# Optimization experiments

Measured on AMD Instinct MI355X. Metric: run time of the kernel, lower is better.

## Reference

```python
import jax, jax.numpy as jnp
import numpy as np

NUM_HEADS = 16


def setup_inputs() -> dict:
    key = jax.random.key(0)
    ks = jax.random.split(key, 7)
    B, S, H = 4, 1024, 1024
    s = 0.02
    return {
        "x": jax.random.normal(ks[0], (B, S, H), dtype=jnp.float32),
        "Wq": jax.random.normal(ks[1], (H, H), dtype=jnp.float32) * s,
        "bq": jax.random.normal(ks[2], (H,), dtype=jnp.float32) * s,
        "Wk": jax.random.normal(ks[3], (H, H), dtype=jnp.float32) * s,
        "bk": jax.random.normal(ks[4], (H,), dtype=jnp.float32) * s,
        "Wv": jax.random.normal(ks[5], (H, H), dtype=jnp.float32) * s,
        "bv": jax.random.normal(ks[6], (H,), dtype=jnp.float32) * s,
    }


def _split_heads(y, num_heads):
    # rearrange 'b s (h c) -> h b s c'
    b, s, hid = y.shape
    c = hid // num_heads
    return y.reshape(b, s, num_heads, c).transpose(2, 0, 1, 3)


def reference(x, Wq, bq, Wk, bk, Wv, bv):
    h = NUM_HEADS
    head_size = x.shape[-1] // h
    # torch Linear: y = x @ W.T + b
    q = _split_heads(x @ Wq.T + bq, h)  # [h,b,s,c]
    k = _split_heads(x @ Wk.T + bk, h)
    v = _split_heads(x @ Wv.T + bv, h)
    scores = jnp.einsum('hbfc,hbtc->hbft', q, k) / jnp.sqrt(
        jnp.asarray(head_size, x.dtype))
    patterns = jax.nn.softmax(scores, axis=-1)  # softmax over t
    # NOTE: faithful to source, contracts over f (query axis) per
    # einsum('hbft,hbfc->hbtc', patterns, value)
    av = jnp.einsum('hbft,hbfc->hbtc', patterns, v)  # [h,b,t,c]
    # rearrange 'h b s c -> b s (c h)'  (channel-major interleave)
    out = av.transpose(1, 2, 3, 0)  # [b,s,c,h]
    b, s, c, hh = out.shape
    return out.reshape(b, s, c * hh)
```

## Files before the change

### kernel.cpp

```cpp
#include <hip/hip_runtime.h>
#include <hip/hip_bf16.h>

typedef short bf16x8 __attribute__((ext_vector_type(8)));
typedef short bf16x4 __attribute__((ext_vector_type(4)));
typedef float f32x4 __attribute__((ext_vector_type(4)));
typedef unsigned short u16;

#define MFMA32(a, b, c) __builtin_amdgcn_mfma_f32_16x16x32_bf16(a, b, c, 0, 0, 0)

#if defined(__has_builtin)
#if __has_builtin(__builtin_amdgcn_mfma_f32_16x16x16bf16_1k)
#define HAVE_MFMA16 1
#define MFMA16(a, b, c) __builtin_amdgcn_mfma_f32_16x16x16bf16_1k(a, b, c, 0, 0, 0)
#endif
#endif
#ifndef HAVE_MFMA16
static __device__ inline f32x4 mfma16_asm(bf16x4 a, bf16x4 b, f32x4 c) {
    f32x4 d;
    asm volatile("v_mfma_f32_16x16x16_bf16 %0, %1, %2, %3\n\ts_nop 7\n\ts_nop 7"
                 : "=v"(d) : "v"(a), "v"(b), "v"(c));
    return d;
}
#define MFMA16(a, b, c) mfma16_asm(a, b, c)
#endif

__device__ inline float fexp2(float x) {
#if defined(__has_builtin) && __has_builtin(__builtin_amdgcn_exp2f)
    return __builtin_amdgcn_exp2f(x);
#else
    return exp2f(x);
#endif
}

__device__ inline u16 f2bf(float f) {
    unsigned u = __float_as_uint(f);
    unsigned r = (u + 0x7fffu + ((u >> 16) & 1u)) >> 16;
    return (u16)r;
}

__device__ inline float bf2f(u16 v) {
    return __uint_as_float(((unsigned)v) << 16);
}

__device__ inline void gload_lds16(const void* g, void* l) {
    __builtin_amdgcn_global_load_lds(
        (const __attribute__((address_space(1))) void*)g,
        (__attribute__((address_space(3))) void*)l, 16, 0, 0);
}

#define BARRIER() __builtin_amdgcn_s_barrier()

__device__ inline int swz(int row, int colbyte) {
    return row * 128 + (colbyte ^ ((row & 7) << 4));
}

__device__ inline void stage8k_512(const u16* __restrict__ g, int gstride,
                                   u16* lds, int tid) {
    int o = tid * 16;
    int row = o >> 7;
    int colb = (o & 127) ^ ((row & 7) << 4);
    gload_lds16(g + row * gstride + (colb >> 1), (char*)lds + o);
}

__device__ inline void stage16k_256(const u16* __restrict__ g, int gstride,
                                    u16* lds, int tid) {
#pragma unroll
    for (int j = 0; j < 4; j++) {
        int o = (tid + j * 256) * 16;
        int row = o >> 7;
        int colb = (o & 127) ^ ((row & 7) << 4);
        gload_lds16(g + row * gstride + (colb >> 1), (char*)lds + o);
    }
}

__global__ void k_convert(const float* __restrict__ src, u16* __restrict__ dst, int n) {
    int i = (blockIdx.x * blockDim.x + threadIdx.x) * 4;
    if (i < n) {
        float4 v = *reinterpret_cast<const float4*>(src + i);
        ushort4 o;
        o.x = f2bf(v.x); o.y = f2bf(v.y); o.z = f2bf(v.z); o.w = f2bf(v.w);
        *reinterpret_cast<ushort4*>(dst + i) = o;
    }
}

__global__ void k_convert3(const float* __restrict__ s0, const float* __restrict__ s1,
                           const float* __restrict__ s2, u16* __restrict__ dst) {
    const float* s = (blockIdx.y == 0) ? s0 : ((blockIdx.y == 1) ? s1 : s2);
    int i = (blockIdx.x * blockDim.x + threadIdx.x) * 4;
    float4 v = *reinterpret_cast<const float4*>(s + i);
    ushort4 o;
    o.x = f2bf(v.x); o.y = f2bf(v.y); o.z = f2bf(v.z); o.w = f2bf(v.w);
    *reinterpret_cast<ushort4*>(dst + blockIdx.y * 1048576 + i) = o;
}

__global__ __launch_bounds__(256, 3) void k_proj(
    const u16* __restrict__ xb, const u16* __restrict__ wb,
    const float* __restrict__ bq, const float* __restrict__ bk, const float* __restrict__ bv,
    u16* __restrict__ outQ, u16* __restrict__ outK, u16* __restrict__ outVt)
{
    __shared__ __align__(16) u16 As[8192];
    __shared__ __align__(16) u16 Bs[8192];
    const int tid = threadIdx.x;
    const int lane = tid & 63;
    const int w = tid >> 6;
    const int bid = blockIdx.x;
    const int xcd = bid & 7, idx = bid >> 3;
    const int mg = xcd & 3, ng = xcd >> 2;
    const int m0 = (mg * 8 + (idx & 7)) * 128;
    const int nfull = ng * 12 + (idx >> 3);
    const int widx = nfull >> 3;
    const int n0 = (nfull & 7) * 128;
    const u16* W = wb + widx * 1024 * 1024;
    const float* bias = (widx == 0) ? bq : ((widx == 1) ? bk : bv);

    const int wm = (w >> 1) * 64, wn = (w & 1) * 64;
    const int lm = lane & 15, lg = lane >> 4;

    f32x4 zero = {0.f, 0.f, 0.f, 0.f};
    f32x4 acc[4][4];
#pragma unroll
    for (int m = 0; m < 4; m++)
#pragma unroll
        for (int n = 0; n < 4; n++) acc[m][n] = zero;

    for (int it = 0; it < 16; ++it) {
        stage16k_256(xb + m0 * 1024 + it * 64, 1024, As, tid);
        stage16k_256(W + n0 * 1024 + it * 64, 1024, Bs, tid);
        __syncthreads();
        const char* Ab = (const char*)As;
        const char* Bb = (const char*)Bs;
#pragma unroll
        for (int kk = 0; kk < 2; kk++) {
            bf16x8 a[4], b[4];
#pragma unroll
            for (int m = 0; m < 4; m++)
                a[m] = *(const bf16x8*)(Ab + swz(wm + m * 16 + lm, kk * 64 + lg * 16));
#pragma unroll
            for (int n = 0; n < 4; n++)
                b[n] = *(const bf16x8*)(Bb + swz(wn + n * 16 + lm, kk * 64 + lg * 16));
#pragma unroll
            for (int m = 0; m < 4; m++)
#pragma unroll
                for (int n = 0; n < 4; n++)
                    acc[m][n] = MFMA32(a[m], b[n], acc[m][n]);
        }
        __syncthreads();
    }

#pragma unroll
    for (int n = 0; n < 4; n++) {
        int col = n0 + wn + n * 16 + lm;
        float bz = bias[col];
        int h = col >> 6, c = col & 63;
#pragma unroll
        for (int m = 0; m < 4; m++) {
#pragma unroll
            for (int r = 0; r < 4; r++) {
                int row = m0 + wm + m * 16 + lg * 4 + r;
                float v = acc[m][n][r] + bz;
                int bb = row >> 10, s = row & 1023;
                int hb = h * 4 + bb;
                if (widx == 0) {
                    outQ[(hb * 1024 + s) * 64 + c] = f2bf(v * 0.18033688011112042f);
                } else if (widx == 1) {
                    outK[(hb * 1024 + s) * 64 + c] = f2bf(v);
                } else {
                    outVt[(hb * 64 + c) * 1024 + s] = f2bf(v);
                }
            }
        }
    }
}

__global__ __launch_bounds__(512, 2) void k_stats(
    const u16* __restrict__ Q, const u16* __restrict__ K, float* __restrict__ linv_out)
{
    __shared__ __align__(16) u16 sK[2][4096];
    const int bid = blockIdx.x;
    const int hb = (bid & 7) * 8 + ((bid >> 3) & 7);
    const int fb = (bid >> 6) * 256;
    const int tid = threadIdx.x, lane = tid & 63, w = tid >> 6;
    const int lm = lane & 15, lg = lane >> 4;
    const u16* Qh = Q + hb * 65536;
    const u16* Kh = K + hb * 65536;

    bf16x8 a[2][2];
#pragma unroll
    for (int fg = 0; fg < 2; fg++) {
        const u16* qp = &Qh[(fb + w * 32 + fg * 16 + lm) * 64 + lg * 8];
        a[fg][0] = *(const bf16x8*)qp;
        a[fg][1] = *(const bf16x8*)(qp + 32);
    }

    float lrun[2][4] = {{0.f, 0.f, 0.f, 0.f}, {0.f, 0.f, 0.f, 0.f}};

    stage8k_512(Kh, 64, sK[0], tid);
    int cur = 0;
    for (int it = 0; it < 16; ++it) {
        if (it < 15) {
            stage8k_512(Kh + (it + 1) * 64 * 64, 64, sK[cur ^ 1], tid);
            asm volatile("s_waitcnt vmcnt(1)" ::: "memory");
        } else {
            asm volatile("s_waitcnt vmcnt(0)" ::: "memory");
        }
        BARRIER();
        const char* base = (const char*)sK[cur];
#pragma unroll
        for (int n = 0; n < 4; n++) {
            int r = n * 16 + lm;
            bf16x8 b0 = *(const bf16x8*)(base + swz(r, lg * 16));
            bf16x8 b1 = *(const bf16x8*)(base + swz(r, 64 + lg * 16));
#pragma unroll
            for (int fg = 0; fg < 2; fg++) {
                f32x4 z = {0.f, 0.f, 0.f, 0.f};
                z = MFMA32(a[fg][0], b0, z);
                z = MFMA32(a[fg][1], b1, z);
                lrun[fg][0] += fexp2(z[0]);
                lrun[fg][1] += fexp2(z[1]);
                lrun[fg][2] += fexp2(z[2]);
                lrun[fg][3] += fexp2(z[3]);
            }
        }
        BARRIER();
        cur ^= 1;
    }
#pragma unroll
    for (int fg = 0; fg < 2; fg++) {
#pragma unroll
        for (int r = 0; r < 4; r++) {
            float s = lrun[fg][r];
            s += __shfl_xor(s, 1);
            s += __shfl_xor(s, 2);
            s += __shfl_xor(s, 4);
            s += __shfl_xor(s, 8);
            if (lm == 0)
                linv_out[hb * 1024 + fb + w * 32 + fg * 16 + lg * 4 + r] = 1.0f / s;
        }
    }
}

__global__ __launch_bounds__(512, 2) void k_av(
    const u16* __restrict__ Q, const u16* __restrict__ K, const u16* __restrict__ Vt,
    const float* __restrict__ linv, u16* __restrict__ av_sb)
{
    __shared__ __align__(16) u16 sQ[2][4096];
    __shared__ __align__(16) u16 sV[2][4096];
    __shared__ __align__(16) float linv_lds[1024];
    const int bid = blockIdx.x;
    const int hb = (bid & 7) * 8 + ((bid >> 3) & 7);
    const int tb = (bid >> 6) * 256;
    const int tid = threadIdx.x, lane = tid & 63, w = tid >> 6;
    const int lm = lane & 15, lg = lane >> 4;
    const u16* Qh = Q + hb * 65536;
    const u16* Kh = K + hb * 65536;
    const u16* Vh = Vt + hb * 65536;
    const float* lh = linv + hb * 1024;

    bf16x8 bK[2][2];
#pragma unroll
    for (int tg = 0; tg < 2; tg++) {
        const u16* kp = &Kh[(tb + w * 32 + tg * 16 + lm) * 64 + lg * 8];
        bK[tg][0] = *(const bf16x8*)kp;
        bK[tg][1] = *(const bf16x8*)(kp + 32);
    }

    f32x4 zero = {0.f, 0.f, 0.f, 0.f};
    f32x4 accv[2][4];
#pragma unroll
    for (int tg = 0; tg < 2; tg++)
#pragma unroll
        for (int m = 0; m < 4; m++) accv[tg][m] = zero;

    stage8k_512(Qh, 64, sQ[0], tid);
    stage8k_512(Vh, 1024, sV[0], tid);
    *reinterpret_cast<float2*>(&linv_lds[tid * 2]) =
        *reinterpret_cast<const float2*>(&lh[tid * 2]);
    __syncthreads();

    int cur = 0;
    for (int it = 0; it < 16; ++it) {
        if (it < 15) {
            int fn = (it + 1) * 64;
            stage8k_512(Qh + fn * 64, 64, sQ[cur ^ 1], tid);
            stage8k_512(Vh + fn, 1024, sV[cur ^ 1], tid);
            asm volatile("s_waitcnt vmcnt(2)" ::: "memory");
        } else {
            asm volatile("s_waitcnt vmcnt(0)" ::: "memory");
        }
        if (it > 0) BARRIER();
        const char* Qb = (const char*)sQ[cur];
        const char* Vb = (const char*)sV[cur];
        const int fc = it * 64;

        bf16x4 afrag[2][4];
#pragma unroll
        for (int mq = 0; mq < 4; mq++) {
            bf16x8 aq0 = *(const bf16x8*)(Qb + swz(mq * 16 + lm, lg * 16));
            bf16x8 aq1 = *(const bf16x8*)(Qb + swz(mq * 16 + lm, 64 + lg * 16));
            float4 lv = *reinterpret_cast<const float4*>(&linv_lds[fc + mq * 16 + lg * 4]);
#pragma unroll
            for (int tg = 0; tg < 2; tg++) {
                f32x4 z = {0.f, 0.f, 0.f, 0.f};
                z = MFMA32(aq0, bK[tg][0], z);
                z = MFMA32(aq1, bK[tg][1], z);
                union { __hip_bfloat162 h2[2]; bf16x4 v4; } u;
                u.h2[0] = __float22bfloat162_rn(
                    make_float2(fexp2(z[0]) * lv.x, fexp2(z[1]) * lv.y));
                u.h2[1] = __float22bfloat162_rn(
                    make_float2(fexp2(z[2]) * lv.z, fexp2(z[3]) * lv.w));
                afrag[tg][mq] = u.v4;
            }
        }
#pragma unroll
        for (int m = 0; m < 4; m++) {
#pragma unroll
            for (int kc = 0; kc < 4; kc++) {
                bf16x4 bv = *(const bf16x4*)(Vb + swz(m * 16 + lm, kc * 32 + lg * 8));
#pragma unroll
                for (int tg = 0; tg < 2; tg++)
                    accv[tg][m] = MFMA16(afrag[tg][kc], bv, accv[tg][m]);
            }
        }
        BARRIER();
        cur ^= 1;
    }

#pragma unroll
    for (int tg = 0; tg < 2; tg++) {
#pragma unroll
        for (int m = 0; m < 4; m++) {
#pragma unroll
            for (int r = 0; r < 4; r++) {
                int t = tb + w * 32 + tg * 16 + lg * 4 + r;
                av_sb[hb * 65536 + t * 64 + m * 16 + lm] = f2bf(accv[tg][m][r]);
            }
        }
    }
}

__global__ __launch_bounds__(256) void k_interleave(
    const u16* __restrict__ av_sb, float* __restrict__ out)
{
    const int bid = blockIdx.x;
    const int bb = bid >> 7, ts = (bid & 127) * 8;
    const int c = threadIdx.x & 63, tl = threadIdx.x >> 6;
#pragma unroll
    for (int p = 0; p < 2; p++) {
        int t = ts + p * 4 + tl;
        float4 w[4];
#pragma unroll
        for (int q = 0; q < 4; q++) {
#pragma unroll
            for (int j = 0; j < 4; j++) {
                int h = q * 4 + j;
                ((float*)&w[q])[j] = bf2f(av_sb[((h * 4 + bb) * 1024 + t) * 64 + c]);
            }
        }
        float4* dst = (float4*)&out[(bb * 1024 + t) * 1024 + c * 16];
        dst[0] = w[0]; dst[1] = w[1]; dst[2] = w[2]; dst[3] = w[3];
    }
}

extern "C" void kernel_launch(void* const* d_in, const int* in_sizes, int n_in,
                              void* d_out, int out_size, void* d_ws, size_t ws_size,
                              hipStream_t stream) {
    const float* x  = (const float*)d_in[0];
    const float* Wq = (const float*)d_in[1];
    const float* bq = (const float*)d_in[2];
    const float* Wk = (const float*)d_in[3];
    const float* bk = (const float*)d_in[4];
    const float* Wv = (const float*)d_in[5];
    const float* bv = (const float*)d_in[6];
    float* out = (float*)d_out;
    char* ws = (char*)d_ws;

    u16* xb = (u16*)ws;
    u16* wb = (u16*)(ws + (8u << 20));
    u16* Qb = (u16*)(ws + (14u << 20));
    u16* Kb = (u16*)(ws + (22u << 20));
    u16* Vt = (u16*)(ws + (30u << 20));
    float* linv = (float*)(ws + (38u << 20));
    u16* av_sb = (u16*)ws;

    k_convert<<<4096, 256, 0, stream>>>(x, xb, 4096 * 1024);
    k_convert3<<<dim3(1024, 3), 256, 0, stream>>>(Wq, Wk, Wv, wb);
    k_proj<<<768, 256, 0, stream>>>(xb, wb, bq, bk, bv, Qb, Kb, Vt);
    k_stats<<<256, 512, 0, stream>>>(Qb, Kb, linv);
    k_av<<<256, 512, 0, stream>>>(Qb, Kb, Vt, linv, av_sb);
    k_interleave<<<512, 256, 0, stream>>>(av_sb, out);
}
```

Before: 103.8 us.

## Merge convert kernels, shrink projection N-tile, set MFMA priority, relayout AV buffer

Merges the x and weight bf16 conversions into one launch. Halves the projection GEMM N-tile to 64 and doubles the grid to 1536 blocks, raising the occupancy hint to 6 so more waves can hide latency. Adds s_setprio around the MFMA loop in the attention-value kernel, and stores AV output in a [b][t][h][c] layout so the interleave kernel reads contiguously. The smaller tile lowers reuse of the A tile and adds more global loads of x per output.

```diff
diff --git a/kernel.cpp b/kernel.cpp
--- a/kernel.cpp
+++ b/kernel.cpp
@@ -73,33 +73,48 @@
     }
 }
 
-__global__ void k_convert(const float* __restrict__ src, u16* __restrict__ dst, int n) {
-    int i = (blockIdx.x * blockDim.x + threadIdx.x) * 4;
-    if (i < n) {
-        float4 v = *reinterpret_cast<const float4*>(src + i);
-        ushort4 o;
-        o.x = f2bf(v.x); o.y = f2bf(v.y); o.z = f2bf(v.z); o.w = f2bf(v.w);
-        *reinterpret_cast<ushort4*>(dst + i) = o;
-    }
-}
-
-__global__ void k_convert3(const float* __restrict__ s0, const float* __restrict__ s1,
-                           const float* __restrict__ s2, u16* __restrict__ dst) {
-    const float* s = (blockIdx.y == 0) ? s0 : ((blockIdx.y == 1) ? s1 : s2);
-    int i = (blockIdx.x * blockDim.x + threadIdx.x) * 4;
+__device__ inline void stage8k_256(const u16* __restrict__ g, int gstride,
+                                   u16* lds, int tid) {
+#pragma unroll
+    for (int j = 0; j < 2; j++) {
+        int o = (tid + j * 256) * 16;
+        int row = o >> 7;
+        int colb = (o & 127) ^ ((row & 7) << 4);
+        gload_lds16(g + row * gstride + (colb >> 1), (char*)lds + o);
+    }
+}
+
+__global__ void k_convert_all(const float* __restrict__ x,
+                              const float* __restrict__ w0, const float* __restrict__ w1,
+                              const float* __restrict__ w2,
+                              u16* __restrict__ xb, u16* __restrict__ wb) {
+    const int bid = blockIdx.x;
+    const float* s;
+    u16* d;
+    int i;
+    if (bid < 4096) {
+        s = x; d = xb;
+        i = bid * 1024 + threadIdx.x * 4;
+    } else {
+        int wsec = (bid - 4096) >> 10;
+        int boff = (bid - 4096) & 1023;
+        s = (wsec == 0) ? w0 : ((wsec == 1) ? w1 : w2);
+        d = wb + wsec * 1048576;
+        i = boff * 1024 + threadIdx.x * 4;
+    }
     float4 v = *reinterpret_cast<const float4*>(s + i);
     ushort4 o;
     o.x = f2bf(v.x); o.y = f2bf(v.y); o.z = f2bf(v.z); o.w = f2bf(v.w);
-    *reinterpret_cast<ushort4*>(dst + blockIdx.y * 1048576 + i) = o;
-}
-
-__global__ __launch_bounds__(256, 3) void k_proj(
+    *reinterpret_cast<ushort4*>(d + i) = o;
+}
+
+__global__ __launch_bounds__(256, 6) void k_proj(
     const u16* __restrict__ xb, const u16* __restrict__ wb,
     const float* __restrict__ bq, const float* __restrict__ bk, const float* __restrict__ bv,
     u16* __restrict__ outQ, u16* __restrict__ outK, u16* __restrict__ outVt)
 {
     __shared__ __align__(16) u16 As[8192];
-    __shared__ __align__(16) u16 Bs[8192];
+    __shared__ __align__(16) u16 Bs[4096];
     const int tid = threadIdx.x;
     const int lane = tid & 63;
     const int w = tid >> 6;
@@ -107,48 +122,48 @@
     const int xcd = bid & 7, idx = bid >> 3;
     const int mg = xcd & 3, ng = xcd >> 2;
     const int m0 = (mg * 8 + (idx & 7)) * 128;
-    const int nfull = ng * 12 + (idx >> 3);
-    const int widx = nfull >> 3;
-    const int n0 = (nfull & 7) * 128;
+    const int nfull = ng * 24 + (idx >> 3);
+    const int widx = nfull >> 4;
+    const int n0 = (nfull & 15) * 64;
     const u16* W = wb + widx * 1024 * 1024;
     const float* bias = (widx == 0) ? bq : ((widx == 1) ? bk : bv);
 
-    const int wm = (w >> 1) * 64, wn = (w & 1) * 64;
+    const int wm = (w >> 1) * 64, wn = (w & 1) * 32;
     const int lm = lane & 15, lg = lane >> 4;
 
     f32x4 zero = {0.f, 0.f, 0.f, 0.f};
-    f32x4 acc[4][4];
+    f32x4 acc[4][2];
 #pragma unroll
     for (int m = 0; m < 4; m++)
 #pragma unroll
-        for (int n = 0; n < 4; n++) acc[m][n] = zero;
+        for (int n = 0; n < 2; n++) acc[m][n] = zero;
 
     for (int it = 0; it < 16; ++it) {
         stage16k_256(xb + m0 * 1024 + it * 64, 1024, As, tid);
-        stage16k_256(W + n0 * 1024 + it * 64, 1024, Bs, tid);
+        stage8k_256(W + n0 * 1024 + it * 64, 1024, Bs, tid);
         __syncthreads();
         const char* Ab = (const char*)As;
         const char* Bb = (const char*)Bs;
 #pragma unroll
         for (int kk = 0; kk < 2; kk++) {
-            bf16x8 a[4], b[4];
+            bf16x8 a[4], b[2];
 #pragma unroll
             for (int m = 0; m < 4; m++)
                 a[m] = *(const bf16x8*)(Ab + swz(wm + m * 16 + lm, kk * 64 + lg * 16));
 #pragma unroll
-            for (int n = 0; n < 4; n++)
+            for (int n = 0; n < 2; n++)
                 b[n] = *(const bf16x8*)(Bb + swz(wn + n * 16 + lm, kk * 64 + lg * 16));
 #pragma unroll
             for (int m = 0; m < 4; m++)
 #pragma unroll
-                for (int n = 0; n < 4; n++)
+                for (int n = 0; n < 2; n++)
                     acc[m][n] = MFMA32(a[m], b[n], acc[m][n]);
         }
         __syncthreads();
     }
 
 #pragma unroll
-    for (int n = 0; n < 4; n++) {
+    for (int n = 0; n < 2; n++) {
         int col = n0 + wn + n * 16 + lm;
         float bz = bias[col];
         int h = col >> 6, c = col & 63;
@@ -311,6 +326,7 @@
                 afrag[tg][mq] = u.v4;
             }
         }
+        __builtin_amdgcn_s_setprio(1);
 #pragma unroll
         for (int m = 0; m < 4; m++) {
 #pragma unroll
@@ -321,10 +337,12 @@
                     accv[tg][m] = MFMA16(afrag[tg][kc], bv, accv[tg][m]);
             }
         }
+        __builtin_amdgcn_s_setprio(0);
         BARRIER();
         cur ^= 1;
     }
 
+    const int h = hb >> 2, bb = hb & 3;
 #pragma unroll
     for (int tg = 0; tg < 2; tg++) {
 #pragma unroll
@@ -332,7 +350,7 @@
 #pragma unroll
             for (int r = 0; r < 4; r++) {
                 int t = tb + w * 32 + tg * 16 + lg * 4 + r;
-                av_sb[hb * 65536 + t * 64 + m * 16 + lm] = f2bf(accv[tg][m][r]);
+                av_sb[((bb * 1024 + t) * 16 + h) * 64 + m * 16 + lm] = f2bf(accv[tg][m][r]);
             }
         }
     }
@@ -347,13 +365,14 @@
 #pragma unroll
     for (int p = 0; p < 2; p++) {
         int t = ts + p * 4 + tl;
+        const u16* src = &av_sb[(bb * 1024 + t) * 1024];
         float4 w[4];
 #pragma unroll
         for (int q = 0; q < 4; q++) {
 #pragma unroll
             for (int j = 0; j < 4; j++) {
                 int h = q * 4 + j;
-                ((float*)&w[q])[j] = bf2f(av_sb[((h * 4 + bb) * 1024 + t) * 64 + c]);
+                ((float*)&w[q])[j] = bf2f(src[h * 64 + c]);
             }
         }
         float4* dst = (float4*)&out[(bb * 1024 + t) * 1024 + c * 16];
@@ -382,9 +401,8 @@
     float* linv = (float*)(ws + (38u << 20));
     u16* av_sb = (u16*)ws;
 
-    k_convert<<<4096, 256, 0, stream>>>(x, xb, 4096 * 1024);
-    k_convert3<<<dim3(1024, 3), 256, 0, stream>>>(Wq, Wk, Wv, wb);
-    k_proj<<<768, 256, 0, stream>>>(xb, wb, bq, bk, bv, Qb, Kb, Vt);
+    k_convert_all<<<7168, 256, 0, stream>>>(x, Wq, Wk, Wv, xb, wb);
+    k_proj<<<1536, 256, 0, stream>>>(xb, wb, bq, bk, bv, Qb, Kb, Vt);
     k_stats<<<256, 512, 0, stream>>>(Qb, Kb, linv);
     k_av<<<256, 512, 0, stream>>>(Qb, Kb, Vt, linv, av_sb);
     k_interleave<<<512, 256, 0, stream>>>(av_sb, out);
```

New measurement: 109.1 us. 5.1% more time.
